# Performance work log

Measured on AMD Instinct MI355X. Metric: run time of the kernel, lower is better.

## Reference

```python
import jax, jax.numpy as jnp
import numpy as np

NQ = 8
DIM = 2 ** NQ  # 256 amplitudes
HALF_PI = float(np.pi / 2)

CNOT_M = jnp.array([[1, 0, 0, 0], [0, 1, 0, 0], [0, 0, 0, 1], [0, 0, 1, 0]], dtype=jnp.complex64)
SWAP_M = jnp.array([[1, 0, 0, 0], [0, 0, 1, 0], [0, 1, 0, 0], [0, 0, 0, 1]], dtype=jnp.complex64)

# PauliZ sign vectors per wire; wire 0 is the most-significant bit (PennyLane convention)
_bits = (np.arange(DIM)[None, :] >> (NQ - 1 - np.arange(NQ))[:, None]) & 1
ZSIGNS = jnp.asarray(1.0 - 2.0 * _bits, dtype=jnp.float32)  # [NQ, DIM]


def _rx(t):
    c = jnp.cos(0.5 * t).astype(jnp.complex64)
    s = (-1j * jnp.sin(0.5 * t)).astype(jnp.complex64)
    return jnp.stack([jnp.stack([c, s]), jnp.stack([s, c])])


def _ry(t):
    c = jnp.cos(0.5 * t).astype(jnp.complex64)
    s = jnp.sin(0.5 * t).astype(jnp.complex64)
    return jnp.stack([jnp.stack([c, -s]), jnp.stack([s, c])])


def _rz(t):
    e0 = jnp.exp(-0.5j * t).astype(jnp.complex64)
    e1 = jnp.exp(0.5j * t).astype(jnp.complex64)
    z = jnp.zeros((), jnp.complex64)
    return jnp.stack([jnp.stack([e0, z]), jnp.stack([z, e1])])


def _ixx(t):
    c = jnp.cos(0.5 * t).astype(jnp.complex64)
    s = (-1j * jnp.sin(0.5 * t)).astype(jnp.complex64)
    z = jnp.zeros((), jnp.complex64)
    return jnp.stack([jnp.stack([c, z, z, s]), jnp.stack([z, c, s, z]),
                      jnp.stack([z, s, c, z]), jnp.stack([s, z, z, c])])


def _apply_1q(psi, U, w):
    # psi: [B] + [2]*NQ ; apply 2x2 U on wire w
    psi = jnp.moveaxis(psi, 1 + w, -1)
    psi = psi @ U.T
    return jnp.moveaxis(psi, -1, 1 + w)


def _apply_2q(psi, U, w1, w2):
    # apply 4x4 U on wires (w1, w2); w1 is the more-significant wire of U
    psi = jnp.moveaxis(psi, (1 + w1, 1 + w2), (-2, -1))
    shp = psi.shape
    psi = (psi.reshape(shp[:-2] + (4,)) @ U.T).reshape(shp)
    return jnp.moveaxis(psi, (-2, -1), (1 + w1, 1 + w2))


def _edges_from_coupling(coupling):
    # Mirrors the torch code: threshold min-max normalized coupling at 0.5.
    # This is a non-differentiable, data-dependent circuit-structure decision,
    # so it is resolved on concrete values (as the Python ifs do in torch).
    c = np.asarray(jax.device_get(coupling), dtype=np.float64)
    cn = (c - c.min()) / (c.max() - c.min())
    adj = cn > 0.5
    return [(i, j) for i in range(NQ) for j in range(i + 1, NQ) if adj[i, j]]


def _conv(psi, i, j, p):
    psi = _apply_1q(psi, _rz(jnp.float32(-HALF_PI)), j)
    psi = _apply_2q(psi, CNOT_M, j, i)  # CNOT control=j target=i
    psi = _apply_1q(psi, _rz(p[0]), i)
    psi = _apply_1q(psi, _ry(p[1]), j)
    psi = _apply_2q(psi, CNOT_M, i, j)
    psi = _apply_1q(psi, _ry(p[2]), j)
    psi = _apply_2q(psi, CNOT_M, j, i)
    psi = _apply_1q(psi, _rz(jnp.float32(HALF_PI)), i)
    return psi


def _pool(psi, i, j, p):
    psi = _apply_1q(psi, _rz(jnp.float32(-HALF_PI)), j)
    psi = _apply_2q(psi, CNOT_M, j, i)
    psi = _apply_1q(psi, _rz(p[0]), i)
    psi = _apply_1q(psi, _ry(p[1]), j)
    psi = _apply_2q(psi, CNOT_M, i, j)
    psi = _apply_1q(psi, _ry(p[2]), j)
    return psi


def _circuit(x, weights, coupling, edges):
    B = x.shape[0]
    # AmplitudeEmbedding(normalize=True)
    psi = (x / jnp.linalg.norm(x, axis=1, keepdims=True)).astype(jnp.complex64)
    psi = psi.reshape((B,) + (2,) * NQ)
    for i in range(NQ):
        psi = _apply_1q(psi, _rx(weights[i]), i)
        psi = _apply_1q(psi, _ry(weights[i + NQ]), i)
        psi = _apply_1q(psi, _rz(weights[i + 2 * NQ]), i)
    for i in range(NQ):
        for j in range(i + 1, NQ):
            psi = _apply_2q(psi, _ixx(coupling[i, j]), i, j)
    widx = 3 * NQ
    for (i, j) in edges:
        nonadjacent = abs(i - j) != 1
        if nonadjacent:
            psi = _apply_2q(psi, SWAP_M, i, j)
        psi = _conv(psi, i, j, weights[widx:widx + 3])
        psi = _pool(psi, i, j, weights[widx + 3:widx + 6])
        widx += 6
        if nonadjacent:
            psi = _apply_2q(psi, SWAP_M, i, j)
    psi_f = psi.reshape(B, DIM)
    probs = psi_f.real ** 2 + psi_f.imag ** 2  # [B, DIM]
    return probs @ ZSIGNS.T  # [B, NQ] expval(PauliZ(i))


def setup_inputs() -> dict:
    B = 65536
    key = jax.random.key(0)
    k1, k2, k3 = jax.random.split(key, 3)
    x = jax.random.normal(k1, (B, DIM), dtype=jnp.float32)
    weights = jax.random.normal(k2, (3 * NQ + 6 * 28,), dtype=jnp.float32)  # 192: max edges = C(8,2)=28
    coupling = jax.random.normal(k3, (NQ, NQ), dtype=jnp.float32)
    return {"x": x, "weights": weights, "coupling": coupling}


def reference(x, weights, coupling):
    edges = _edges_from_coupling(coupling)
    return _circuit(x, weights, coupling, edges)
```

## Files before the change

kernel.cpp:

```cpp
#include <hip/hip_runtime.h>

#define HP 1.57079632679489662f

typedef float f32x4 __attribute__((ext_vector_type(4)));
typedef short sh4 __attribute__((ext_vector_type(4)));

__device__ __forceinline__ unsigned short f2bf(float f) {
  unsigned int u = __builtin_bit_cast(unsigned int, f);
  u += 0x7fffu + ((u >> 16) & 1u);
  return (unsigned short)(u >> 16);
}

__device__ __forceinline__ void rowswap4(float (&mr)[4][4], float (&mi)[4][4], int a, int b) {
#pragma unroll
  for (int c = 0; c < 4; c++) {
    float tr = mr[a][c]; mr[a][c] = mr[b][c]; mr[b][c] = tr;
    float ti = mi[a][c]; mi[a][c] = mi[b][c]; mi[b][c] = ti;
  }
}

__device__ __forceinline__ void absorb_rz(float (&mr)[4][4], float (&mi)[4][4], float t, int bitpos) {
  float ch = cosf(0.5f * t), sh = sinf(0.5f * t);
#pragma unroll
  for (int r = 0; r < 4; r++) {
    float ph = ((r >> bitpos) & 1) ? sh : -sh;
#pragma unroll
    for (int c = 0; c < 4; c++) {
      float ar = mr[r][c], ai = mi[r][c];
      mr[r][c] = ch * ar - ph * ai;
      mi[r][c] = ch * ai + ph * ar;
    }
  }
}

__device__ __forceinline__ void absorb_ry(float (&mr)[4][4], float (&mi)[4][4], float t, int bitpos) {
  float ch = cosf(0.5f * t), sh = sinf(0.5f * t);
#pragma unroll
  for (int r = 0; r < 4; r++) {
    if ((r >> bitpos) & 1) continue;
    int rb = r | (1 << bitpos);
#pragma unroll
    for (int c = 0; c < 4; c++) {
      float ar = mr[r][c], ai = mi[r][c];
      float br = mr[rb][c], bi = mi[rb][c];
      mr[r][c]  = ch * ar - sh * br;  mi[r][c]  = ch * ai - sh * bi;
      mr[rb][c] = sh * ar + ch * br;  mi[rb][c] = sh * ai + ch * bi;
    }
  }
}


__global__ __launch_bounds__(64) void prep_kernel(const float* __restrict__ wt,
                                                  const float* __restrict__ coup,
                                                  void* __restrict__ wsv) {
  const int lane = threadIdx.x;
  int* meta  = (int*)wsv;
  float* Q1  = (float*)((char*)wsv + 256);
  float* E4  = (float*)((char*)wsv + 512);

  double mn = 1e300, mx = -1e300;
  for (int k = 0; k < 64; k++) {
    double v = (double)coup[k];
    mn = v < mn ? v : mn;
    mx = v > mx ? v : mx;
  }
  int cnt = 0, myi = -1, myj = -1;
  for (int i = 0; i < 8; i++)
    for (int j = i + 1; j < 8; j++) {
      double cn = ((double)coup[i * 8 + j] - mn) / (mx - mn);
      if (cn > 0.5) {
        if (cnt == lane) { myi = i; myj = j; }
        cnt++;
      }
    }
  if (lane == 0) meta[0] = cnt;

  if (lane < 8) {
    float tx = wt[lane], ty = wt[8 + lane], tz = wt[16 + lane];
    float cx = cosf(0.5f * tx), sx = sinf(0.5f * tx);
    float cy = cosf(0.5f * ty), sy = sinf(0.5f * ty);
    float cz = cosf(0.5f * tz), sz = sinf(0.5f * tz);
    float m00r = cy * cx,  m00i = sy * sx;
    float m01r = -sy * cx, m01i = -cy * sx;
    float m10r = sy * cx,  m10i = -cy * sx;
    float m11r = cy * cx,  m11i = -sy * sx;
    float* q = Q1 + lane * 8;
    q[0] = cz * m00r + sz * m00i; q[1] = cz * m00i - sz * m00r;
    q[2] = cz * m01r + sz * m01i; q[3] = cz * m01i - sz * m01r;
    q[4] = cz * m10r - sz * m10i; q[5] = cz * m10i + sz * m10r;
    q[6] = cz * m11r - sz * m11i; q[7] = cz * m11i + sz * m11r;
  }

  if (lane < cnt && lane < 28) {
    float mr[4][4], mi[4][4];
#pragma unroll
    for (int r = 0; r < 4; r++)
#pragma unroll
      for (int c = 0; c < 4; c++) { mr[r][c] = (r == c) ? 1.f : 0.f; mi[r][c] = 0.f; }

    bool nonadj = (myj - myi) != 1;
    int wb = 24 + 6 * lane;

    if (nonadj) rowswap4(mr, mi, 1, 2);
    absorb_rz(mr, mi, -HP, 0);
    rowswap4(mr, mi, 1, 3);
    absorb_rz(mr, mi, wt[wb + 0], 1);
    absorb_ry(mr, mi, wt[wb + 1], 0);
    rowswap4(mr, mi, 2, 3);
    absorb_ry(mr, mi, wt[wb + 2], 0);
    rowswap4(mr, mi, 1, 3);
    absorb_rz(mr, mi, HP, 1);
    absorb_rz(mr, mi, -HP, 0);
    rowswap4(mr, mi, 1, 3);
    absorb_rz(mr, mi, wt[wb + 3], 1);
    absorb_ry(mr, mi, wt[wb + 4], 0);
    rowswap4(mr, mi, 2, 3);
    absorb_ry(mr, mi, wt[wb + 5], 0);
    if (nonadj) rowswap4(mr, mi, 1, 2);

    float* e = E4 + lane * 32;
#pragma unroll
    for (int r = 0; r < 4; r++)
#pragma unroll
      for (int c = 0; c < 4; c++) {
        e[(r * 4 + c) * 2]     = mr[r][c];
        e[(r * 4 + c) * 2 + 1] = mi[r][c];
      }
    meta[1 + 2 * lane] = myi;
    meta[2 + 2 * lane] = myj;
  }
}

__global__ __launch_bounds__(256) void build_u_kernel(const float* __restrict__ coup,
                                                      void* __restrict__ wsv) {
  const int* meta = (const int*)wsv;
  const float* Q1 = (const float*)((char*)wsv + 256);
  const float* E4 = (const float*)((char*)wsv + 512);
  unsigned char* Ub = (unsigned char*)wsv + 4096;

  const int c = blockIdx.x;
  const int tid = threadIdx.x;

  __shared__ float2 s[256];
  s[tid] = make_float2(tid == c ? 1.f : 0.f, 0.f);
  __syncthreads();

  for (int wi = 0; wi < 8; wi++) {
    const float* M = Q1 + wi * 8;
    int p = 7 - wi;
    float2 a0 = s[tid & ~(1 << p)];
    float2 a1 = s[tid | (1 << p)];
    int b = (tid >> p) & 1;
    float m0r = M[(b * 2 + 0) * 2], m0i = M[(b * 2 + 0) * 2 + 1];
    float m1r = M[(b * 2 + 1) * 2], m1i = M[(b * 2 + 1) * 2 + 1];
    float nr = m0r * a0.x - m0i * a0.y + m1r * a1.x - m1i * a1.y;
    float ni = m0r * a0.y + m0i * a0.x + m1r * a1.y + m1i * a1.x;
    __syncthreads();
    s[tid] = make_float2(nr, ni);
    __syncthreads();
  }

  for (int i = 0; i < 8; i++)
    for (int j = i + 1; j < 8; j++) {
      float t = coup[i * 8 + j];
      float ch = cosf(0.5f * t), sn = sinf(0.5f * t);
      int mask = (1 << (7 - i)) | (1 << (7 - j));
      float2 a = s[tid];
      float2 b = s[tid ^ mask];
      __syncthreads();
      s[tid] = make_float2(ch * a.x + sn * b.y, ch * a.y - sn * b.x);
      __syncthreads();
    }

  int ne = meta[0];
  for (int e = 0; e < ne; e++) {
    int i = meta[1 + 2 * e], j = meta[2 + 2 * e];
    int p1 = 7 - i, p2 = 7 - j;
    int m1 = 1 << p1, m2 = 1 << p2;
    int b = ((tid >> p1) & 1) * 2 + ((tid >> p2) & 1);
    int base = tid & ~(m1 | m2);
    float2 a0 = s[base];
    float2 a1 = s[base | m2];
    float2 a2 = s[base | m1];
    float2 a3 = s[base | m1 | m2];
    const float* M = E4 + e * 32 + b * 8;
    float nr = M[0] * a0.x - M[1] * a0.y + M[2] * a1.x - M[3] * a1.y
             + M[4] * a2.x - M[5] * a2.y + M[6] * a3.x - M[7] * a3.y;
    float ni = M[0] * a0.y + M[1] * a0.x + M[2] * a1.y + M[3] * a1.x
             + M[4] * a2.y + M[5] * a2.x + M[6] * a3.y + M[7] * a3.x;
    __syncthreads();
    s[tid] = make_float2(nr, ni);
    __syncthreads();
  }

  {
    int ks = c >> 5, kc = c & 31;
    int sub = kc >> 3, j2 = kc & 7;
    int p = (sub + tid) & 3;
    unsigned char* base = Ub + (size_t)ks * 32768 + (size_t)(2 * tid) * 64 + p * 16 + j2 * 2;
    *(unsigned short*)(base)      = f2bf(s[tid].x);
    *(unsigned short*)(base + 64) = f2bf(s[tid].y);
  }
}

__global__ __launch_bounds__(512) void gemm_mfma16(const float* __restrict__ x,
                                                   const void* __restrict__ wsv,
                                                   float* __restrict__ out) {
  const unsigned char* Ub = (const unsigned char*)wsv + 4096;
  __shared__ __align__(16) unsigned char smem[65536];
  const int AOFF = 32768;

  const int tid = threadIdx.x;
  const int blk = blockIdx.x;
  const int wv = tid >> 6;
  const int lane = tid & 63;
  const int lm = lane & 15;
  const int lg = lane >> 4;

  {
    const int rl = tid >> 3;
    const int seg = tid & 7;
    const float4* xs = (const float4*)(x + (size_t)(blk * 64 + rl) * 256 + seg * 32);
    float4 v[8];
    float ss = 0.f;
#pragma unroll
    for (int i = 0; i < 8; i++) {
      v[i] = xs[i];
      ss += v[i].x * v[i].x + v[i].y * v[i].y + v[i].z * v[i].z + v[i].w * v[i].w;
    }
    ss += __shfl_xor(ss, 1);
    ss += __shfl_xor(ss, 2);
    ss += __shfl_xor(ss, 4);
    float inv = 1.0f / sqrtf(ss);
#pragma unroll
    for (int u = 0; u < 4; u++) {
      unsigned short h[8];
#pragma unroll
      for (int k = 0; k < 8; k++) {
        float f = ((const float*)v)[u * 8 + k] * inv;
        h[k] = f2bf(f);
      }
      uint4 pack;
      pack.x = (unsigned)h[0] | ((unsigned)h[1] << 16);
      pack.y = (unsigned)h[2] | ((unsigned)h[3] << 16);
      pack.z = (unsigned)h[4] | ((unsigned)h[5] << 16);
      pack.w = (unsigned)h[6] | ((unsigned)h[7] << 16);
      int byte = (rl * 512 + seg * 64 + u * 16) ^ ((rl & 7) << 4);
      *reinterpret_cast<uint4*>(&smem[byte]) = pack;
    }
  }

  f32x4 acc[4][4] = {};

  for (int ks = 0; ks < 8; ks++) {
    {
      const uint4* src = (const uint4*)(Ub + (size_t)ks * 32768);
#pragma unroll
      for (int g = 0; g < 4; g++)
        *reinterpret_cast<uint4*>(&smem[AOFF + g * 8192 + tid * 16]) = src[g * 512 + tid];
    }
    __syncthreads();

    sh4 a16[4][2], b16[4][2];
#pragma unroll
    for (int mf = 0; mf < 4; mf++) {
      const int m = wv * 64 + mf * 16 + lm;
#pragma unroll
      for (int h = 0; h < 2; h++) {
        int p = (2 * h + (lg >> 1) + (m >> 1)) & 3;
        a16[mf][h] = __builtin_bit_cast(sh4,
            *reinterpret_cast<const uint2*>(&smem[AOFF + m * 64 + p * 16 + (lg & 1) * 8]));
      }
    }
#pragma unroll
    for (int nf = 0; nf < 4; nf++) {
      const int n = nf * 16 + lm;
#pragma unroll
      for (int h = 0; h < 2; h++) {
        int byte = (n * 512 + ks * 64 + 32 * h + 8 * lg) ^ ((n & 7) << 4);
        b16[nf][h] = __builtin_bit_cast(sh4, *reinterpret_cast<const uint2*>(&smem[byte]));
      }
    }
#pragma unroll
    for (int mf = 0; mf < 4; mf++)
#pragma unroll
      for (int nf = 0; nf < 4; nf++) {
        acc[mf][nf] = __builtin_amdgcn_mfma_f32_16x16x16bf16_1k(a16[mf][0], b16[nf][0], acc[mf][nf], 0, 0, 0);
        acc[mf][nf] = __builtin_amdgcn_mfma_f32_16x16x16bf16_1k(a16[mf][1], b16[nf][1], acc[mf][nf], 0, 0, 0);
      }
    __syncthreads();
  }

  float pq[4][8];
#pragma unroll
  for (int nf = 0; nf < 4; nf++) {
    float T = 0.f, S7 = 0.f, S4 = 0.f, S3 = 0.f;
#pragma unroll
    for (int mf = 0; mf < 4; mf++) {
      f32x4 a = acc[mf][nf];
      float p0 = a[0] * a[0] + a[1] * a[1];
      float p1 = a[2] * a[2] + a[3] * a[3];
      float sp = p0 + p1, d = p0 - p1;
      T += sp;
      S7 += d;
      S4 += (mf & 1) ? -sp : sp;
      S3 += (mf & 2) ? -sp : sp;
    }
    pq[nf][7] = S7;
    pq[nf][6] = (lg & 1) ? -T : T;
    pq[nf][5] = (lg & 2) ? -T : T;
    pq[nf][4] = S4;
    pq[nf][3] = S3;
    pq[nf][2] = (wv & 1) ? -T : T;
    pq[nf][1] = (wv & 2) ? -T : T;
    pq[nf][0] = (wv & 4) ? -T : T;
  }
#pragma unroll
  for (int nf = 0; nf < 4; nf++)
#pragma unroll
    for (int k = 0; k < 8; k++) {
      pq[nf][k] += __shfl_xor(pq[nf][k], 16);
      pq[nf][k] += __shfl_xor(pq[nf][k], 32);
    }

  float* part = (float*)smem;
  if (lg == 0) {
#pragma unroll
    for (int nf = 0; nf < 4; nf++) {
      float* dst = part + (wv * 64 + nf * 16 + lm) * 8;
#pragma unroll
      for (int k = 0; k < 8; k++) dst[k] = pq[nf][k];
    }
  }
  __syncthreads();
  {
    int b = tid >> 3, q = tid & 7;
    float v = 0.f;
#pragma unroll
    for (int w2 = 0; w2 < 8; w2++) v += part[(w2 * 64 + b) * 8 + q];
    out[(size_t)(blk * 64 + b) * 8 + q] = v;
  }
}

extern "C" void kernel_launch(void* const* d_in, const int* in_sizes, int n_in,
                              void* d_out, int out_size, void* d_ws, size_t ws_size,
                              hipStream_t stream) {
  const float* x    = (const float*)d_in[0];
  const float* wt   = (const float*)d_in[1];
  const float* coup = (const float*)d_in[2];
  float* out = (float*)d_out;

  prep_kernel<<<1, 64, 0, stream>>>(wt, coup, d_ws);
  build_u_kernel<<<256, 256, 0, stream>>>(coup, d_ws);
  gemm_mfma16<<<1024, 512, 0, stream>>>(x, d_ws, out);
}
```

Baseline: 72.06 us.

## Keep unitary fragments in registers and loop four batch tiles per block

```diff
diff --git a/kernel.cpp b/kernel.cpp
--- a/kernel.cpp
+++ b/kernel.cpp
@@ -195,150 +195,149 @@
 
   {
     int ks = c >> 5, kc = c & 31;
-    int sub = kc >> 3, j2 = kc & 7;
-    int p = (sub + tid) & 3;
-    unsigned char* base = Ub + (size_t)ks * 32768 + (size_t)(2 * tid) * 64 + p * 16 + j2 * 2;
+    int sb = (kc >> 4) & 1, lg2 = (kc >> 2) & 3, ii = kc & 3;
+    int p = (lg2 + tid) & 3;
+    unsigned char* base = Ub + (size_t)ks * 32768 + (size_t)(2 * tid) * 64 + p * 16 + sb * 8 + ii * 2;
     *(unsigned short*)(base)      = f2bf(s[tid].x);
     *(unsigned short*)(base + 64) = f2bf(s[tid].y);
   }
 }
 
-__global__ __launch_bounds__(512) void gemm_mfma16(const float* __restrict__ x,
-                                                   const void* __restrict__ wsv,
-                                                   float* __restrict__ out) {
+__global__ __launch_bounds__(512, 2) void gemm_persist(const float* __restrict__ x,
+                                                       const void* __restrict__ wsv,
+                                                       float* __restrict__ out) {
   const unsigned char* Ub = (const unsigned char*)wsv + 4096;
-  __shared__ __align__(16) unsigned char smem[65536];
-  const int AOFF = 32768;
+  __shared__ __align__(16) unsigned char smem[32768];
 
   const int tid = threadIdx.x;
-  const int blk = blockIdx.x;
+  const int bid = blockIdx.x;
   const int wv = tid >> 6;
   const int lane = tid & 63;
   const int lm = lane & 15;
   const int lg = lane >> 4;
 
-  {
-    const int rl = tid >> 3;
-    const int seg = tid & 7;
-    const float4* xs = (const float4*)(x + (size_t)(blk * 64 + rl) * 256 + seg * 32);
-    float4 v[8];
-    float ss = 0.f;
-#pragma unroll
-    for (int i = 0; i < 8; i++) {
-      v[i] = xs[i];
-      ss += v[i].x * v[i].x + v[i].y * v[i].y + v[i].z * v[i].z + v[i].w * v[i].w;
-    }
-    ss += __shfl_xor(ss, 1);
-    ss += __shfl_xor(ss, 2);
-    ss += __shfl_xor(ss, 4);
-    float inv = 1.0f / sqrtf(ss);
-#pragma unroll
-    for (int u = 0; u < 4; u++) {
-      unsigned short h[8];
+  uint4 a_st[4][8];
+#pragma unroll
+  for (int mf = 0; mf < 4; mf++) {
+    const int m = wv * 64 + mf * 16 + lm;
+    const int p = (lg + (m >> 1)) & 3;
+#pragma unroll
+    for (int ks = 0; ks < 8; ks++)
+      a_st[mf][ks] = *reinterpret_cast<const uint4*>(Ub + (size_t)ks * 32768 + (size_t)m * 64 + p * 16);
+  }
+
+  for (int t = 0; t < 4; t++) {
+    const int tile = bid * 4 + t;
+
+    {
+      const int rl = tid >> 3;
+      const int seg = tid & 7;
+      const float4* xs = (const float4*)(x + (size_t)(tile * 64 + rl) * 256 + seg * 32);
+      float4 v[8];
+      float ss = 0.f;
+#pragma unroll
+      for (int i = 0; i < 8; i++) {
+        v[i] = xs[i];
+        ss += v[i].x * v[i].x + v[i].y * v[i].y + v[i].z * v[i].z + v[i].w * v[i].w;
+      }
+      ss += __shfl_xor(ss, 1);
+      ss += __shfl_xor(ss, 2);
+      ss += __shfl_xor(ss, 4);
+      float inv = 1.0f / sqrtf(ss);
+      const float* vf = (const float*)v;
+#pragma unroll
+      for (int u = 0; u < 4; u++) {
+        unsigned short h[8];
+#pragma unroll
+        for (int j = 0; j < 8; j++)
+          h[j] = f2bf(vf[16 * (j >> 2) + 4 * u + (j & 3)] * inv);
+        uint4 pack;
+        pack.x = (unsigned)h[0] | ((unsigned)h[1] << 16);
+        pack.y = (unsigned)h[2] | ((unsigned)h[3] << 16);
+        pack.z = (unsigned)h[4] | ((unsigned)h[5] << 16);
+        pack.w = (unsigned)h[6] | ((unsigned)h[7] << 16);
+        int byte = (rl * 512 + seg * 64 + u * 16) ^ ((rl & 7) << 4);
+        *reinterpret_cast<uint4*>(&smem[byte]) = pack;
+      }
+    }
+    __syncthreads();
+
+    f32x4 acc[4][4] = {};
+#pragma unroll
+    for (int ks = 0; ks < 8; ks++) {
+      uint4 bq[4];
+#pragma unroll
+      for (int nf = 0; nf < 4; nf++) {
+        const int n = nf * 16 + lm;
+        int byte = (n * 512 + ks * 64 + lg * 16) ^ ((lm & 7) << 4);
+        bq[nf] = *reinterpret_cast<const uint4*>(&smem[byte]);
+      }
+#pragma unroll
+      for (int mf = 0; mf < 4; mf++) {
+        const uint4 aq = a_st[mf][ks];
+        const sh4 alo = __builtin_bit_cast(sh4, make_uint2(aq.x, aq.y));
+        const sh4 ahi = __builtin_bit_cast(sh4, make_uint2(aq.z, aq.w));
+#pragma unroll
+        for (int nf = 0; nf < 4; nf++) {
+          const sh4 blo = __builtin_bit_cast(sh4, make_uint2(bq[nf].x, bq[nf].y));
+          const sh4 bhi = __builtin_bit_cast(sh4, make_uint2(bq[nf].z, bq[nf].w));
+          acc[mf][nf] = __builtin_amdgcn_mfma_f32_16x16x16bf16_1k(alo, blo, acc[mf][nf], 0, 0, 0);
+          acc[mf][nf] = __builtin_amdgcn_mfma_f32_16x16x16bf16_1k(ahi, bhi, acc[mf][nf], 0, 0, 0);
+        }
+      }
+    }
+    __syncthreads();
+
+    float pq[4][8];
+#pragma unroll
+    for (int nf = 0; nf < 4; nf++) {
+      float T = 0.f, S7 = 0.f, S4 = 0.f, S3 = 0.f;
+#pragma unroll
+      for (int mf = 0; mf < 4; mf++) {
+        f32x4 a = acc[mf][nf];
+        float p0 = a[0] * a[0] + a[1] * a[1];
+        float p1 = a[2] * a[2] + a[3] * a[3];
+        float sp = p0 + p1, d = p0 - p1;
+        T += sp;
+        S7 += d;
+        S4 += (mf & 1) ? -sp : sp;
+        S3 += (mf & 2) ? -sp : sp;
+      }
+      pq[nf][7] = S7;
+      pq[nf][6] = (lg & 1) ? -T : T;
+      pq[nf][5] = (lg & 2) ? -T : T;
+      pq[nf][4] = S4;
+      pq[nf][3] = S3;
+      pq[nf][2] = (wv & 1) ? -T : T;
+      pq[nf][1] = (wv & 2) ? -T : T;
+      pq[nf][0] = (wv & 4) ? -T : T;
+    }
+#pragma unroll
+    for (int nf = 0; nf < 4; nf++)
 #pragma unroll
       for (int k = 0; k < 8; k++) {
-        float f = ((const float*)v)[u * 8 + k] * inv;
-        h[k] = f2bf(f);
-      }
-      uint4 pack;
-      pack.x = (unsigned)h[0] | ((unsigned)h[1] << 16);
-      pack.y = (unsigned)h[2] | ((unsigned)h[3] << 16);
-      pack.z = (unsigned)h[4] | ((unsigned)h[5] << 16);
-      pack.w = (unsigned)h[6] | ((unsigned)h[7] << 16);
-      int byte = (rl * 512 + seg * 64 + u * 16) ^ ((rl & 7) << 4);
-      *reinterpret_cast<uint4*>(&smem[byte]) = pack;
-    }
-  }
-
-  f32x4 acc[4][4] = {};
-
-  for (int ks = 0; ks < 8; ks++) {
+        pq[nf][k] += __shfl_xor(pq[nf][k], 16);
+        pq[nf][k] += __shfl_xor(pq[nf][k], 32);
+      }
+
+    float* part = (float*)smem;
+    if (lg == 0) {
+#pragma unroll
+      for (int nf = 0; nf < 4; nf++) {
+        float* dst = part + (wv * 64 + nf * 16 + lm) * 8;
+#pragma unroll
+        for (int k = 0; k < 8; k++) dst[k] = pq[nf][k];
+      }
+    }
+    __syncthreads();
     {
-      const uint4* src = (const uint4*)(Ub + (size_t)ks * 32768);
-#pragma unroll
-      for (int g = 0; g < 4; g++)
-        *reinterpret_cast<uint4*>(&smem[AOFF + g * 8192 + tid * 16]) = src[g * 512 + tid];
-    }
-    __syncthreads();
-
-    sh4 a16[4][2], b16[4][2];
-#pragma unroll
-    for (int mf = 0; mf < 4; mf++) {
-      const int m = wv * 64 + mf * 16 + lm;
-#pragma unroll
-      for (int h = 0; h < 2; h++) {
-        int p = (2 * h + (lg >> 1) + (m >> 1)) & 3;
-        a16[mf][h] = __builtin_bit_cast(sh4,
-            *reinterpret_cast<const uint2*>(&smem[AOFF + m * 64 + p * 16 + (lg & 1) * 8]));
-      }
-    }
-#pragma unroll
-    for (int nf = 0; nf < 4; nf++) {
-      const int n = nf * 16 + lm;
-#pragma unroll
-      for (int h = 0; h < 2; h++) {
-        int byte = (n * 512 + ks * 64 + 32 * h + 8 * lg) ^ ((n & 7) << 4);
-        b16[nf][h] = __builtin_bit_cast(sh4, *reinterpret_cast<const uint2*>(&smem[byte]));
-      }
-    }
-#pragma unroll
-    for (int mf = 0; mf < 4; mf++)
-#pragma unroll
-      for (int nf = 0; nf < 4; nf++) {
-        acc[mf][nf] = __builtin_amdgcn_mfma_f32_16x16x16bf16_1k(a16[mf][0], b16[nf][0], acc[mf][nf], 0, 0, 0);
-        acc[mf][nf] = __builtin_amdgcn_mfma_f32_16x16x16bf16_1k(a16[mf][1], b16[nf][1], acc[mf][nf], 0, 0, 0);
-      }
-    __syncthreads();
-  }
-
-  float pq[4][8];
-#pragma unroll
-  for (int nf = 0; nf < 4; nf++) {
-    float T = 0.f, S7 = 0.f, S4 = 0.f, S3 = 0.f;
-#pragma unroll
-    for (int mf = 0; mf < 4; mf++) {
-      f32x4 a = acc[mf][nf];
-      float p0 = a[0] * a[0] + a[1] * a[1];
-      float p1 = a[2] * a[2] + a[3] * a[3];
-      float sp = p0 + p1, d = p0 - p1;
-      T += sp;
-      S7 += d;
-      S4 += (mf & 1) ? -sp : sp;
-      S3 += (mf & 2) ? -sp : sp;
-    }
-    pq[nf][7] = S7;
-    pq[nf][6] = (lg & 1) ? -T : T;
-    pq[nf][5] = (lg & 2) ? -T : T;
-    pq[nf][4] = S4;
-    pq[nf][3] = S3;
-    pq[nf][2] = (wv & 1) ? -T : T;
-    pq[nf][1] = (wv & 2) ? -T : T;
-    pq[nf][0] = (wv & 4) ? -T : T;
-  }
-#pragma unroll
-  for (int nf = 0; nf < 4; nf++)
-#pragma unroll
-    for (int k = 0; k < 8; k++) {
-      pq[nf][k] += __shfl_xor(pq[nf][k], 16);
-      pq[nf][k] += __shfl_xor(pq[nf][k], 32);
-    }
-
-  float* part = (float*)smem;
-  if (lg == 0) {
-#pragma unroll
-    for (int nf = 0; nf < 4; nf++) {
-      float* dst = part + (wv * 64 + nf * 16 + lm) * 8;
-#pragma unroll
-      for (int k = 0; k < 8; k++) dst[k] = pq[nf][k];
-    }
-  }
-  __syncthreads();
-  {
-    int b = tid >> 3, q = tid & 7;
-    float v = 0.f;
-#pragma unroll
-    for (int w2 = 0; w2 < 8; w2++) v += part[(w2 * 64 + b) * 8 + q];
-    out[(size_t)(blk * 64 + b) * 8 + q] = v;
+      int b = tid >> 3, q = tid & 7;
+      float v2 = 0.f;
+#pragma unroll
+      for (int w2 = 0; w2 < 8; w2++) v2 += part[(w2 * 64 + b) * 8 + q];
+      out[(size_t)(tile * 64 + b) * 8 + q] = v2;
+    }
+    __syncthreads();
   }
 }
 
@@ -352,5 +351,5 @@
 
   prep_kernel<<<1, 64, 0, stream>>>(wt, coup, d_ws);
   build_u_kernel<<<256, 256, 0, stream>>>(coup, d_ws);
-  gemm_mfma16<<<1024, 512, 0, stream>>>(x, d_ws, out);
-}
+  gemm_persist<<<256, 512, 0, stream>>>(x, d_ws, out);
+}
```

New measurement: 75.24 us. 4.4% more time.
